# Performance work log

Hardware: AMD Instinct MI355X
Metric: run time of the kernel (lower is better)

Reference implementation:

```python
import jax, jax.numpy as jnp
import numpy as np

B, T, D = 1, 4096, 2048
NUM_HEADS, NUM_KV_HEADS, HEAD_DIM = 16, 8, 128
QUERY_PRE_ATTN_SCALAR = HEAD_DIM ** -0.5
SOFT_CAP = 50.0
WINDOW = 1024
ROPE_BASE = 10000.0
ROPE_SCALE = 1.0
K_MASK = -2.3819763e+38


def apply_rope(x, positions, head_dim, max_wavelength=ROPE_BASE, scale_factor=ROPE_SCALE):
    # x: [B, T, N, H], positions: [B, T]
    fraction = 2.0 * jnp.arange(head_dim // 2, dtype=jnp.float32) / head_dim
    timescale = max_wavelength ** fraction  # [H/2]
    sinusoid = positions[..., None].astype(jnp.float32) / timescale  # [B, T, H/2]
    sinusoid = (sinusoid / scale_factor)[..., None, :]  # [B, T, 1, H/2]
    sin, cos = jnp.sin(sinusoid), jnp.cos(sinusoid)
    first, second = jnp.split(x, 2, axis=-1)
    out = jnp.concatenate([first * cos - second * sin,
                           second * cos + first * sin], axis=-1)
    return out.astype(x.dtype)


def setup_inputs() -> dict:
    key = jax.random.key(0)
    ks = jax.random.split(key, 4)
    x = jax.random.normal(ks[0], (B, T, D), dtype=jnp.float32)
    segment_pos = jnp.broadcast_to(jnp.arange(T, dtype=jnp.int32), (B, T))
    # causal mask [B, T, S]
    attn_mask = jnp.broadcast_to(
        jnp.tril(jnp.ones((T, T), dtype=jnp.bool_)), (B, T, T))
    q_w = jax.random.normal(ks[1], (NUM_HEADS, D, HEAD_DIM), dtype=jnp.float32) * 0.02
    kv_w = jax.random.normal(ks[2], (2, NUM_KV_HEADS, D, HEAD_DIM), dtype=jnp.float32) * 0.02
    o_w = jax.random.normal(ks[3], (NUM_HEADS, HEAD_DIM, D), dtype=jnp.float32) * 0.02
    return {"x": x, "segment_pos": segment_pos, "attn_mask": attn_mask,
            "q_w": q_w, "kv_w": kv_w, "o_w": o_w}


def reference(x, segment_pos, attn_mask, q_w, kv_w, o_w):
    # Projections (GQA: separate q and kv einsums)
    q = jnp.einsum('BTD,NDH->BTNH', x, q_w)          # [B,T,N,H]
    k = jnp.einsum('BSD,KDH->BSKH', x, kv_w[0])      # [B,S,K,H]
    v = jnp.einsum('BSD,KDH->BSKH', x, kv_w[1])      # [B,S,K,H]

    q = apply_rope(q, segment_pos, HEAD_DIM)
    q = q * QUERY_PRE_ATTN_SCALAR
    k = apply_rope(k, segment_pos, HEAD_DIM)

    num_groups = NUM_HEADS // NUM_KV_HEADS
    qg = q.reshape(B, T, NUM_KV_HEADS, num_groups, HEAD_DIM)
    logits = jnp.einsum('BTKGH,BSKH->BTKGS', qg, k)
    logits = logits.reshape(B, T, NUM_HEADS, -1)     # [B,T,N,S]

    # soft cap
    logits = jnp.tanh(logits / SOFT_CAP) * SOFT_CAP

    # sliding-window mask combined with causal mask
    all_ones = jnp.ones_like(attn_mask)
    sliding = jnp.triu(all_ones, -WINDOW + 1) * jnp.tril(all_ones, WINDOW - 1)
    mask = sliding * attn_mask                       # [B,T,S] bool

    padded = jnp.where(mask[:, :, None, :], logits, K_MASK)
    probs = jax.nn.softmax(padded, axis=-1).astype(k.dtype)

    probs_g = probs.reshape(B, T, NUM_KV_HEADS, num_groups, -1)
    encoded = jnp.einsum('BTKGS,BSKH->BTKGH', probs_g, v)
    encoded = encoded.reshape(B, T, NUM_HEADS, HEAD_DIM)

    attn_output = jnp.einsum('BTNH,NHD->BTD', encoded, o_w)
    return attn_output
```

## Files before the change

### kernel.cpp

```cpp
#include <hip/hip_runtime.h>
#include <hip/hip_bf16.h>
#include <math.h>

typedef __attribute__((ext_vector_type(8))) short short8;
typedef __attribute__((ext_vector_type(8))) unsigned short ushort8;
typedef __attribute__((ext_vector_type(4))) float f32x4;

#define T_SEQ 4096
#define D_MODEL 2048
#define N_HEADS 16
#define N_KV 8
#define HEAD_DIM 128
#define QSCALE 0.08838834764831845f

__device__ __forceinline__ float bf2f(unsigned short u) {
  union { unsigned int i; float f; } x; x.i = ((unsigned int)u) << 16; return x.f;
}
__device__ __forceinline__ unsigned short f2bf(float f) {
  union { float f; unsigned int i; } x; x.f = f;
  unsigned int i = x.i;
  unsigned int r = i + 0x7fffu + ((i >> 16) & 1u);
  return (unsigned short)(r >> 16);
}

__global__ __launch_bounds__(256) void prep_kernel(const float* __restrict__ x,
                                                   unsigned short* __restrict__ xb,
                                                   const int* __restrict__ segpos,
                                                   float2* __restrict__ tab) {
  int b = blockIdx.x;
  if (b < 4096) {
    int idx = b * 256 + threadIdx.x;
    const float4* p = reinterpret_cast<const float4*>(x) + (size_t)idx * 2;
    float4 a = p[0], c = p[1];
    ushort8 o;
    o[0] = f2bf(a.x); o[1] = f2bf(a.y); o[2] = f2bf(a.z); o[3] = f2bf(a.w);
    o[4] = f2bf(c.x); o[5] = f2bf(c.y); o[6] = f2bf(c.z); o[7] = f2bf(c.w);
    reinterpret_cast<ushort8*>(xb)[idx] = o;
  } else {
    int idx = (b - 4096) * 256 + threadIdx.x;
    int t = idx >> 6, i = idx & 63;
    float pos = (float)segpos[t];
    float ts = powf(10000.f, (float)(2 * i) / 128.f);
    float ang = pos / ts;
    tab[idx] = make_float2(sinf(ang), cosf(ang));
  }
}

__global__ __launch_bounds__(256) void wqkv_transpose_kernel(const float* __restrict__ q_w,
                                                             const float* __restrict__ kv_w,
                                                             unsigned short* __restrict__ Wt) {
  __shared__ float tile[32][33];
  int z = blockIdx.z;
  const float* src = (z < 16) ? q_w + (size_t)z * 2048 * 128
                              : kv_w + (size_t)(z - 16) * 2048 * 128;
  unsigned short* dst = Wt + (size_t)z * 128 * 2048;
  int c0 = blockIdx.x * 32, r0 = blockIdx.y * 32;
  int tx = threadIdx.x & 31, ty = threadIdx.x >> 5;
#pragma unroll
  for (int i = 0; i < 4; ++i)
    tile[ty + i * 8][tx] = src[(size_t)(r0 + ty + i * 8) * 128 + c0 + tx];
  __syncthreads();
#pragma unroll
  for (int i = 0; i < 4; ++i)
    dst[(size_t)(c0 + ty + i * 8) * 2048 + r0 + tx] = f2bf(tile[tx][ty + i * 8]);
}

__global__ __launch_bounds__(256) void ow_transpose_kernel(const float* __restrict__ src,
                                                           unsigned short* __restrict__ dst) {
  __shared__ float tile[32][33];
  int c0 = blockIdx.x * 32, r0 = blockIdx.y * 32;
  int tx = threadIdx.x & 31, ty = threadIdx.x >> 5;
#pragma unroll
  for (int i = 0; i < 4; ++i)
    tile[ty + i * 8][tx] = src[(size_t)(r0 + ty + i * 8) * 2048 + c0 + tx];
  __syncthreads();
#pragma unroll
  for (int i = 0; i < 4; ++i)
    dst[(size_t)(c0 + ty + i * 8) * 2048 + r0 + tx] = f2bf(tile[tx][ty + i * 8]);
}

#define G2L(gp, lp)                                                           \
  __builtin_amdgcn_global_load_lds(                                           \
      (const __attribute__((address_space(1))) void*)(gp),                    \
      (__attribute__((address_space(3))) void*)(lp), 16, 0, 0)
#define GBAR() asm volatile("s_barrier" ::: "memory")
#define VMW(n) asm volatile("s_waitcnt vmcnt(" #n ")" ::: "memory")

template <int OUT_BF16, int NHB>
__global__ __launch_bounds__(512, 2) void gemm256_kernel(const unsigned short* __restrict__ A,
                                                         const unsigned short* __restrict__ Bt,
                                                         void* __restrict__ Cout,
                                                         int M, int N, int K) {
  constexpr int NW = 2 * NHB;
  extern __shared__ unsigned short smem[];
  unsigned short* ldsA = smem;
  unsigned short* ldsB = smem + 32768;
  const int tid = threadIdx.x;
  const int lane = tid & 63, wave = tid >> 6;
  const int wm = wave >> 2, wn = wave & 3;
  const int lr = lane & 15, lg = lane >> 4;
  const int swz = (lr & 7) << 3;
  const int c0s = (lg * 8) ^ swz;
  const int c1s = (32 + lg * 8) ^ swz;

  int id = blockIdx.y * gridDim.x + blockIdx.x;
  int nb = gridDim.x * gridDim.y;
  int sw = (id & 7) * (nb >> 3) + (id >> 3);
  const long brow = (long)(sw / gridDim.x) * 256;
  const long bcol = (long)(sw % gridDim.x) * (128 * NHB);

  const unsigned short* Ag = A + brow * K;
  const unsigned short* Bg = Bt + bcol * K;

  const int r0 = tid >> 3;
  const int cs = ((tid & 7) * 8) ^ ((r0 & 7) << 3);

#define ST_A(tt, b, a)                                                        \
  { G2L(Ag + (size_t)((a) * 128 + r0) * K + (size_t)(tt) * 64 + cs,           \
        ldsA + (b) * 16384 + (a) * 8192 + tid * 8);                           \
    G2L(Ag + (size_t)((a) * 128 + r0 + 64) * K + (size_t)(tt) * 64 + cs,      \
        ldsA + (b) * 16384 + (a) * 8192 + 4096 + tid * 8); }
#define ST_B(tt, b, h)                                                        \
  { G2L(Bg + (size_t)((h) * 128 + r0) * K + (size_t)(tt) * 64 + cs,           \
        ldsB + (b) * 8192 * NHB + (h) * 8192 + tid * 8);                      \
    G2L(Bg + (size_t)((h) * 128 + r0 + 64) * K + (size_t)(tt) * 64 + cs,      \
        ldsB + (b) * 8192 * NHB + (h) * 8192 + 4096 + tid * 8); }

  f32x4 acc[8][NW] = {};
  short8 bf[NW][2];
  short8 af[4];

#define RD_B(b)                                                               \
  { const unsigned short* pb = ldsB + (b) * 8192 * NHB + wn * 2048 * NHB;     \
    _Pragma("unroll")                                                         \
    for (int n = 0; n < NW; ++n) {                                            \
      bf[n][0] = *(const short8*)(pb + (n * 16 + lr) * 64 + c0s);             \
      bf[n][1] = *(const short8*)(pb + (n * 16 + lr) * 64 + c1s);             \
    } }
#define RD_A(b, mb)                                                           \
  { const unsigned short* pa = ldsA + (b) * 16384 + wm * 8192;                \
    af[0] = *(const short8*)(pa + ((mb) * 16 + lr) * 64 + c0s);               \
    af[1] = *(const short8*)(pa + ((mb) * 16 + lr) * 64 + c1s);               \
    af[2] = *(const short8*)(pa + ((mb) * 16 + 16 + lr) * 64 + c0s);          \
    af[3] = *(const short8*)(pa + ((mb) * 16 + 16 + lr) * 64 + c1s); }
#define MFMA2(mb)                                                             \
  { __builtin_amdgcn_s_setprio(1);                                            \
    _Pragma("unroll")                                                         \
    for (int n = 0; n < NW; ++n) {                                            \
      acc[mb][n]     = __builtin_amdgcn_mfma_f32_16x16x32_bf16(af[0], bf[n][0], acc[mb][n], 0, 0, 0);     \
      acc[mb][n]     = __builtin_amdgcn_mfma_f32_16x16x32_bf16(af[1], bf[n][1], acc[mb][n], 0, 0, 0);     \
      acc[mb + 1][n] = __builtin_amdgcn_mfma_f32_16x16x32_bf16(af[2], bf[n][0], acc[mb + 1][n], 0, 0, 0); \
      acc[mb + 1][n] = __builtin_amdgcn_mfma_f32_16x16x32_bf16(af[3], bf[n][1], acc[mb + 1][n], 0, 0, 0); \
    }                                                                         \
    __builtin_amdgcn_s_setprio(0); }

  ST_B(0, 0, 0);
  if constexpr (NHB == 2) ST_B(0, 0, 1);
  ST_A(0, 0, 0); ST_A(0, 0, 1);
  ST_B(1, 1, 0);
  if constexpr (NHB == 2) ST_B(1, 1, 1);
  if constexpr (NHB == 2) { VMW(4); } else { VMW(2); }
  ST_A(1, 1, 0); ST_A(1, 1, 1);
  GBAR();

  const int NT = K >> 6;
  for (int j = 0; j < (NT >> 1); ++j) {
    const int t2 = 2 * j + 2, t3 = 2 * j + 3;
    const bool s2 = t2 < NT, s3 = t3 < NT;
    RD_B(0); RD_A(0, 0);
    if (s2) ST_B(t2, 0, 0);
    GBAR(); MFMA2(0); GBAR();
    RD_A(0, 2);
    if constexpr (NHB == 2) { if (s2) ST_B(t2, 0, 1); }
    GBAR(); MFMA2(2); GBAR();
    RD_A(0, 4);
    GBAR(); MFMA2(4); GBAR();
    RD_A(0, 6);
    if (s2) {
      if constexpr (NHB == 2) { VMW(4); } else { VMW(2); }
      ST_A(t2, 0, 0); ST_A(t2, 0, 1);
    } else { VMW(0); }
    GBAR(); MFMA2(6); GBAR();
    RD_B(1); RD_A(1, 0);
    if (s3) ST_B(t3, 1, 0);
    GBAR(); MFMA2(0); GBAR();
    RD_A(1, 2);
    if constexpr (NHB == 2) { if (s3) ST_B(t3, 1, 1); }
    GBAR(); MFMA2(2); GBAR();
    RD_A(1, 4);
    GBAR(); MFMA2(4); GBAR();
    RD_A(1, 6);
    if (s3) {
      if constexpr (NHB == 2) { VMW(4); } else { VMW(2); }
      ST_A(t3, 1, 0); ST_A(t3, 1, 1);
    } else { VMW(0); }
    GBAR(); MFMA2(6); GBAR();
  }

#undef ST_A
#undef ST_B
#undef RD_A
#undef RD_B
#undef MFMA2

#pragma unroll
  for (int m = 0; m < 8; ++m) {
#pragma unroll
    for (int i = 0; i < 4; ++i) {
      long row = brow + wm * 128 + m * 16 + lg * 4 + i;
#pragma unroll
      for (int n = 0; n < NW; ++n) {
        long col = bcol + wn * (32 * NHB) + n * 16 + lr;
        if (OUT_BF16)
          ((unsigned short*)Cout)[row * N + col] = f2bf(acc[m][n][i]);
        else
          ((float*)Cout)[row * N + col] = acc[m][n][i];
      }
    }
  }
}

__global__ __launch_bounds__(256) void rope_vt_kernel(const unsigned short* __restrict__ raw,
                                                      const float2* __restrict__ tab,
                                                      unsigned short* __restrict__ Qb,
                                                      unsigned short* __restrict__ Kb,
                                                      unsigned short* __restrict__ Vt) {
  __shared__ unsigned short tile[32][33];
  int b = blockIdx.x;
  if (b < 3072) {
    int gid = b * 256 + threadIdx.x;
    int j = gid & 7;
    int rem = gid >> 3;
    int hs = rem % 24;
    int t = rem / 24;
    int i0 = j * 8;
    float sv[8], cv[8];
    const float2* tp = tab + t * 64 + i0;
#pragma unroll
    for (int q = 0; q < 8; ++q) { float2 sc2 = tp[q]; sv[q] = sc2.x; cv[q] = sc2.y; }
    if (hs < 16) {
      const unsigned short* p = raw + (size_t)t * 4096 + hs * 128 + i0;
      ushort8 a = *(const ushort8*)p;
      ushort8 c = *(const ushort8*)(p + 64);
      ushort8 o1, o2;
#pragma unroll
      for (int q = 0; q < 8; ++q) {
        float fa = bf2f(a[q]), fb = bf2f(c[q]);
        o1[q] = f2bf((fa * cv[q] - fb * sv[q]) * QSCALE);
        o2[q] = f2bf((fb * cv[q] + fa * sv[q]) * QSCALE);
      }
      unsigned short* qp = Qb + ((size_t)hs * T_SEQ + t) * 128 + i0;
      *(ushort8*)qp = o1;
      *(ushort8*)(qp + 64) = o2;
    } else {
      int kn = hs - 16;
      const unsigned short* p = raw + (size_t)t * 4096 + 2048 + kn * 128 + i0;
      ushort8 a = *(const ushort8*)p;
      ushort8 c = *(const ushort8*)(p + 64);
      ushort8 o1, o2;
#pragma unroll
      for (int q = 0; q < 8; ++q) {
        float fa = bf2f(a[q]), fb = bf2f(c[q]);
        o1[q] = f2bf(fa * cv[q] - fb * sv[q]);
        o2[q] = f2bf(fb * cv[q] + fa * sv[q]);
      }
      unsigned short* kp = Kb + ((size_t)kn * T_SEQ + t) * 128 + i0;
      *(ushort8*)kp = o1;
      *(ushort8*)(kp + 64) = o2;
    }
  } else {
    int id = b - 3072;
    int bx = id & 3, by = (id >> 2) & 127, bz = id >> 9;
    const unsigned short* src = raw + 3072 + (size_t)bz * 128;
    unsigned short* dst = Vt + (size_t)bz * 128 * 4096;
    int c0 = bx * 32, r0 = by * 32;
    int tx = threadIdx.x & 31, ty = threadIdx.x >> 5;
#pragma unroll
    for (int i = 0; i < 4; ++i)
      tile[ty + i * 8][tx] = src[(size_t)(r0 + ty + i * 8) * 4096 + c0 + tx];
    __syncthreads();
#pragma unroll
    for (int i = 0; i < 4; ++i)
      dst[(size_t)(c0 + ty + i * 8) * 4096 + r0 + tx] = tile[tx][ty + i * 8];
  }
}

__global__ __launch_bounds__(256, 4) void attn_kernel(const unsigned short* __restrict__ Qb,
                                                      const unsigned short* __restrict__ Kb,
                                                      const unsigned short* __restrict__ Vt,
                                                      unsigned short* __restrict__ enc) {
  __shared__ unsigned short Ks[64][128];
  __shared__ unsigned short Vs[128][64];
  __shared__ unsigned short Ps[4][16][72];
  int rawb = blockIdx.y * 64 + blockIdx.x;
  int lin = (rawb & 7) * 128 + (rawb >> 3);
  const int h = lin >> 6;
  const int qb0 = (lin & 63) * 64;
  const int kvh = h >> 1;
  const int tid = threadIdx.x, lane = tid & 63, wave = tid >> 6;
  const int qw = qb0 + wave * 16;
  const int lr = lane & 15, lg = lane >> 4;
  const int sw = (lr & 7) << 3;

  short8 aq[4];
  {
    const unsigned short* qp = Qb + ((size_t)h * T_SEQ + qw + lr) * 128 + lg * 8;
#pragma unroll
    for (int c = 0; c < 4; ++c) aq[c] = *(const short8*)(qp + c * 32);
  }
  f32x4 acc[8] = {};
  float lsum = 0.f;

  const int s_lo = (qb0 - 1023) > 0 ? (qb0 - 1023) : 0;
  const int kb_lo = s_lo >> 6, kb_hi = (qb0 + 63) >> 6;

  const int rK = tid >> 4;
  const int cpK = (tid & 15) * 8;
  const int colK = cpK ^ ((rK & 7) << 3);
  const int rV = tid >> 3;
  const int cpV = (tid & 7) * 8;
  const int colV = cpV ^ ((rV & 7) << 3);
  const unsigned short* kgb = Kb + ((size_t)kvh * T_SEQ + rK) * 128 + colK;
  const unsigned short* vgb = Vt + ((size_t)kvh * 128 + rV) * T_SEQ + colV;

  ushort8 kr[4], vr[4];
  {
    const int s0g = kb_lo * 64;
#pragma unroll
    for (int j = 0; j < 4; ++j) {
      kr[j] = *(const ushort8*)(kgb + (size_t)(s0g + j * 16) * 128);
      vr[j] = *(const ushort8*)(vgb + (size_t)(j * 32) * T_SEQ + s0g);
    }
  }

  const int qg = qw + lr;
  for (int kb = kb_lo; kb <= kb_hi; ++kb) {
    const int s0g = kb * 64;
    __syncthreads();
#pragma unroll
    for (int j = 0; j < 4; ++j) {
      *(ushort8*)&Ks[rK + j * 16][cpK] = kr[j];
      *(ushort8*)&Vs[rV + j * 32][cpV] = vr[j];
    }
    __syncthreads();
    if (kb < kb_hi) {
      const int sn = s0g + 64;
#pragma unroll
      for (int j = 0; j < 4; ++j) {
        kr[j] = *(const ushort8*)(kgb + (size_t)(sn + j * 16) * 128);
        vr[j] = *(const ushort8*)(vgb + (size_t)(j * 32) * T_SEQ + sn);
      }
    }
    if (s0g > qw + 15 || s0g + 63 < qw - 1023) continue;
    const bool interior = (s0g + 63 <= qw) && (s0g >= qw - 1008);

    f32x4 sT[4] = {};
    __builtin_amdgcn_s_setprio(1);
#pragma unroll
    for (int st = 0; st < 4; ++st) {
      const int krow = st * 16 + lr;
#pragma unroll
      for (int c = 0; c < 4; ++c) {
        short8 kf = *(const short8*)&Ks[krow][(c * 32 + lg * 8) ^ sw];
        sT[st] = __builtin_amdgcn_mfma_f32_16x16x32_bf16(kf, aq[c], sT[st], 0, 0, 0);
      }
    }
    __builtin_amdgcn_s_setprio(0);
#pragma unroll
    for (int st = 0; st < 4; ++st) {
      float p[4];
#pragma unroll
      for (int r = 0; r < 4; ++r) {
        float s = sT[st][r];
        float sl = s * 1.44269504f;
        float z2 = s * s * 4.0e-4f;
        float e = sl * (15.f + z2) * __builtin_amdgcn_rcpf(fmaf(z2, 6.f, 15.f));
        if (!interior) {
          int sg = s0g + st * 16 + lg * 4 + r;
          e = ((unsigned)(qg - sg) <= 1023u) ? e : -__builtin_inff();
        }
        float pv;
        asm("v_exp_f32 %0, %1" : "=v"(pv) : "v"(e));
        lsum += pv;
        p[r] = pv;
      }
      unsigned u0, u1;
      asm("v_cvt_pk_bf16_f32 %0, %1, %2" : "=v"(u0) : "v"(p[0]), "v"(p[1]));
      asm("v_cvt_pk_bf16_f32 %0, %1, %2" : "=v"(u1) : "v"(p[2]), "v"(p[3]));
      uint2 w; w.x = u0; w.y = u1;
      *(uint2*)&Ps[wave][lr][st * 16 + lg * 4] = w;
    }
    short8 pa0 = *(const short8*)&Ps[wave][lr][lg * 8];
    short8 pa1 = *(const short8*)&Ps[wave][lr][32 + lg * 8];
    __builtin_amdgcn_s_setprio(1);
#pragma unroll
    for (int d0 = 0; d0 < 8; ++d0) {
      const int vrow = d0 * 16 + lr;
      short8 bv0 = *(const short8*)&Vs[vrow][(lg * 8) ^ sw];
      short8 bv1 = *(const short8*)&Vs[vrow][(32 + lg * 8) ^ sw];
      acc[d0] = __builtin_amdgcn_mfma_f32_16x16x32_bf16(pa0, bv0, acc[d0], 0, 0, 0);
      acc[d0] = __builtin_amdgcn_mfma_f32_16x16x32_bf16(pa1, bv1, acc[d0], 0, 0, 0);
    }
    __builtin_amdgcn_s_setprio(0);
  }

  float l = lsum;
  l += __shfl_xor(l, 16);
  l += __shfl_xor(l, 32);
#pragma unroll
  for (int r = 0; r < 4; ++r) {
    float lt = __shfl(l, lg * 4 + r);
    float inv = __builtin_amdgcn_rcpf(lt);
    int row = qw + lg * 4 + r;
    unsigned short* op = enc + (size_t)row * D_MODEL + h * 128 + lr;
#pragma unroll
    for (int d0 = 0; d0 < 8; ++d0) op[d0 * 16] = f2bf(acc[d0][r] * inv);
  }
}

extern "C" void kernel_launch(void* const* d_in, const int* in_sizes, int n_in,
                              void* d_out, int out_size, void* d_ws, size_t ws_size,
                              hipStream_t stream) {
  const float* x = (const float*)d_in[0];
  const int* segpos = (const int*)d_in[1];
  const float* q_w = (const float*)d_in[3];
  const float* kv_w = (const float*)d_in[4];
  const float* o_w = (const float*)d_in[5];
  float* out = (float*)d_out;
  char* ws = (char*)d_ws;

  const size_t OFF_XB = 0;
  const size_t OFF_WT = OFF_XB + 16777216;
  const size_t OFF_RAW = OFF_WT + 16777216;
  const size_t OFF_KB = OFF_RAW + 33554432;
  const size_t OFF_VT = OFF_KB + 8388608;
  const size_t OFF_TAB = OFF_VT + 8388608;
  unsigned short* xb = (unsigned short*)(ws + OFF_XB);
  unsigned short* Wt = (unsigned short*)(ws + OFF_WT);
  unsigned short* raw = (unsigned short*)(ws + OFF_RAW);
  unsigned short* Kb = (unsigned short*)(ws + OFF_KB);
  unsigned short* Vt = (unsigned short*)(ws + OFF_VT);
  float2* tab = (float2*)(ws + OFF_TAB);
  unsigned short* o_wt = xb;
  unsigned short* Qb = Wt;
  unsigned short* enc = raw;

  hipFuncSetAttribute((const void*)(gemm256_kernel<1, 2>),
                      hipFuncAttributeMaxDynamicSharedMemorySize, 131072);
  hipFuncSetAttribute((const void*)(gemm256_kernel<0, 1>),
                      hipFuncAttributeMaxDynamicSharedMemorySize, 98304);

  prep_kernel<<<dim3(5120), dim3(256), 0, stream>>>(x, xb, segpos, tab);
  wqkv_transpose_kernel<<<dim3(4, 64, 32), dim3(256), 0, stream>>>(q_w, kv_w, Wt);
  gemm256_kernel<1, 2><<<dim3(16, 16), dim3(512), 131072, stream>>>(xb, Wt, (void*)raw, 4096, 4096, 2048);
  ow_transpose_kernel<<<dim3(64, 64), dim3(256), 0, stream>>>(o_w, o_wt);
  rope_vt_kernel<<<dim3(7168), dim3(256), 0, stream>>>(raw, tab, Qb, Kb, Vt);
  attn_kernel<<<dim3(64, 16), dim3(256), 0, stream>>>(Qb, Kb, Vt, enc);
  gemm256_kernel<0, 1><<<dim3(16, 16), dim3(512), 98304, stream>>>(enc, o_wt, (void*)out, 4096, 2048, 2048);
}
```

Before: 211.9 us.

## Enlarge attention query tile per block and retile GEMM to 128x256

The attention kernel now runs 512-thread blocks over 256 query rows, and each wave handles two 16-row query groups. That lets each K/V fragment read from LDS feed twice as many MFMAs and cuts redundant K/V global loads across blocks. The GEMM template switches its parameter from N-halves to M-halves, so the output projection uses 128x256 tiles with a restructured pipeline that adds explicit lgkmcnt waits. The softcap and exp math is also vectorised into float2 form. The cost is higher register pressure and fewer, larger attention blocks (256), which may leave the load less balanced across CUs.

```diff
diff --git a/kernel.cpp b/kernel.cpp
--- a/kernel.cpp
+++ b/kernel.cpp
@@ -5,6 +5,7 @@
 typedef __attribute__((ext_vector_type(8))) short short8;
 typedef __attribute__((ext_vector_type(8))) unsigned short ushort8;
 typedef __attribute__((ext_vector_type(4))) float f32x4;
+typedef __attribute__((ext_vector_type(2))) float f32x2;
 
 #define T_SEQ 4096
 #define D_MODEL 2048
@@ -85,16 +86,18 @@
       (__attribute__((address_space(3))) void*)(lp), 16, 0, 0)
 #define GBAR() asm volatile("s_barrier" ::: "memory")
 #define VMW(n) asm volatile("s_waitcnt vmcnt(" #n ")" ::: "memory")
-
-template <int OUT_BF16, int NHB>
+#define LGKM0()                                                               \
+  { asm volatile("s_waitcnt lgkmcnt(0)" ::: "memory");                        \
+    __builtin_amdgcn_sched_barrier(0); }
+
+template <int OUT_BF16, int MHB>
 __global__ __launch_bounds__(512, 2) void gemm256_kernel(const unsigned short* __restrict__ A,
                                                          const unsigned short* __restrict__ Bt,
                                                          void* __restrict__ Cout,
                                                          int M, int N, int K) {
-  constexpr int NW = 2 * NHB;
   extern __shared__ unsigned short smem[];
   unsigned short* ldsA = smem;
-  unsigned short* ldsB = smem + 32768;
+  unsigned short* ldsB = smem + 2 * MHB * 8192;
   const int tid = threadIdx.x;
   const int lane = tid & 63, wave = tid >> 6;
   const int wm = wave >> 2, wn = wave & 3;
@@ -106,8 +109,8 @@
   int id = blockIdx.y * gridDim.x + blockIdx.x;
   int nb = gridDim.x * gridDim.y;
   int sw = (id & 7) * (nb >> 3) + (id >> 3);
-  const long brow = (long)(sw / gridDim.x) * 256;
-  const long bcol = (long)(sw % gridDim.x) * (128 * NHB);
+  const long brow = (long)(sw / gridDim.x) * (128 * MHB);
+  const long bcol = (long)(sw % gridDim.x) * 256;
 
   const unsigned short* Ag = A + brow * K;
   const unsigned short* Bg = Bt + bcol * K;
@@ -117,28 +120,28 @@
 
 #define ST_A(tt, b, a)                                                        \
   { G2L(Ag + (size_t)((a) * 128 + r0) * K + (size_t)(tt) * 64 + cs,           \
-        ldsA + (b) * 16384 + (a) * 8192 + tid * 8);                           \
+        ldsA + (b) * (MHB * 8192) + (a) * 8192 + tid * 8);                    \
     G2L(Ag + (size_t)((a) * 128 + r0 + 64) * K + (size_t)(tt) * 64 + cs,      \
-        ldsA + (b) * 16384 + (a) * 8192 + 4096 + tid * 8); }
+        ldsA + (b) * (MHB * 8192) + (a) * 8192 + 4096 + tid * 8); }
 #define ST_B(tt, b, h)                                                        \
   { G2L(Bg + (size_t)((h) * 128 + r0) * K + (size_t)(tt) * 64 + cs,           \
-        ldsB + (b) * 8192 * NHB + (h) * 8192 + tid * 8);                      \
+        ldsB + (b) * 16384 + (h) * 8192 + tid * 8);                           \
     G2L(Bg + (size_t)((h) * 128 + r0 + 64) * K + (size_t)(tt) * 64 + cs,      \
-        ldsB + (b) * 8192 * NHB + (h) * 8192 + 4096 + tid * 8); }
-
-  f32x4 acc[8][NW] = {};
-  short8 bf[NW][2];
+        ldsB + (b) * 16384 + (h) * 8192 + 4096 + tid * 8); }
+
+  f32x4 acc[4 * MHB][4] = {};
+  short8 bf[4][2];
   short8 af[4];
 
 #define RD_B(b)                                                               \
-  { const unsigned short* pb = ldsB + (b) * 8192 * NHB + wn * 2048 * NHB;     \
+  { const unsigned short* pb = ldsB + (b) * 16384 + wn * 4096;                \
     _Pragma("unroll")                                                         \
-    for (int n = 0; n < NW; ++n) {                                            \
+    for (int n = 0; n < 4; ++n) {                                             \
       bf[n][0] = *(const short8*)(pb + (n * 16 + lr) * 64 + c0s);             \
       bf[n][1] = *(const short8*)(pb + (n * 16 + lr) * 64 + c1s);             \
     } }
 #define RD_A(b, mb)                                                           \
-  { const unsigned short* pa = ldsA + (b) * 16384 + wm * 8192;                \
+  { const unsigned short* pa = ldsA + (b) * (MHB * 8192) + wm * (MHB * 4096); \
     af[0] = *(const short8*)(pa + ((mb) * 16 + lr) * 64 + c0s);               \
     af[1] = *(const short8*)(pa + ((mb) * 16 + lr) * 64 + c1s);               \
     af[2] = *(const short8*)(pa + ((mb) * 16 + 16 + lr) * 64 + c0s);          \
@@ -146,7 +149,7 @@
 #define MFMA2(mb)                                                             \
   { __builtin_amdgcn_s_setprio(1);                                            \
     _Pragma("unroll")                                                         \
-    for (int n = 0; n < NW; ++n) {                                            \
+    for (int n = 0; n < 4; ++n) {                                             \
       acc[mb][n]     = __builtin_amdgcn_mfma_f32_16x16x32_bf16(af[0], bf[n][0], acc[mb][n], 0, 0, 0);     \
       acc[mb][n]     = __builtin_amdgcn_mfma_f32_16x16x32_bf16(af[1], bf[n][1], acc[mb][n], 0, 0, 0);     \
       acc[mb + 1][n] = __builtin_amdgcn_mfma_f32_16x16x32_bf16(af[2], bf[n][0], acc[mb + 1][n], 0, 0, 0); \
@@ -154,49 +157,47 @@
     }                                                                         \
     __builtin_amdgcn_s_setprio(0); }
 
-  ST_B(0, 0, 0);
-  if constexpr (NHB == 2) ST_B(0, 0, 1);
-  ST_A(0, 0, 0); ST_A(0, 0, 1);
-  ST_B(1, 1, 0);
-  if constexpr (NHB == 2) ST_B(1, 1, 1);
-  if constexpr (NHB == 2) { VMW(4); } else { VMW(2); }
-  ST_A(1, 1, 0); ST_A(1, 1, 1);
+  ST_B(0, 0, 0); ST_B(0, 0, 1);
+  ST_A(0, 0, 0);
+  if constexpr (MHB == 2) ST_A(0, 0, 1);
+  ST_B(1, 1, 0); ST_B(1, 1, 1);
+  if constexpr (MHB == 2) { VMW(4); } else { VMW(4); }
+  ST_A(1, 1, 0);
+  if constexpr (MHB == 2) ST_A(1, 1, 1);
   GBAR();
+
+#define TILE(b, tn, sflag)                                                    \
+  { RD_B(b); RD_A(b, 0);                                                      \
+    LGKM0(); GBAR();                \
+    if (sflag) ST_B(tn, b, 0);                 \
+    MFMA2(0); GBAR();                                                         \
+    if constexpr (MHB == 1) {                                                 \
+      RD_A(b, 2);                                                             \
+      LGKM0(); GBAR();                          \
+      if (sflag) { ST_B(tn, b, 1); VMW(4); ST_A(tn, b, 0); }                  \
+      else       { VMW(0); }                                                  \
+      MFMA2(2); GBAR();                                                       \
+    } else {                                                                  \
+      RD_A(b, 2);                                                             \
+      if (sflag) ST_B(tn, b, 1);         \
+      GBAR(); MFMA2(2); GBAR();                                               \
+      RD_A(b, 4);                                                             \
+      GBAR(); MFMA2(4); GBAR();                                               \
+      RD_A(b, 6);                                                             \
+      LGKM0(); GBAR();                          \
+      if (sflag) { VMW(4); ST_A(tn, b, 0); ST_A(tn, b, 1); }                  \
+      else       { VMW(0); }                                                  \
+      MFMA2(6); GBAR();                                                       \
+    } }
 
   const int NT = K >> 6;
   for (int j = 0; j < (NT >> 1); ++j) {
     const int t2 = 2 * j + 2, t3 = 2 * j + 3;
-    const bool s2 = t2 < NT, s3 = t3 < NT;
-    RD_B(0); RD_A(0, 0);
-    if (s2) ST_B(t2, 0, 0);
-    GBAR(); MFMA2(0); GBAR();
-    RD_A(0, 2);
-    if constexpr (NHB == 2) { if (s2) ST_B(t2, 0, 1); }
-    GBAR(); MFMA2(2); GBAR();
-    RD_A(0, 4);
-    GBAR(); MFMA2(4); GBAR();
-    RD_A(0, 6);
-    if (s2) {
-      if constexpr (NHB == 2) { VMW(4); } else { VMW(2); }
-      ST_A(t2, 0, 0); ST_A(t2, 0, 1);
-    } else { VMW(0); }
-    GBAR(); MFMA2(6); GBAR();
-    RD_B(1); RD_A(1, 0);
-    if (s3) ST_B(t3, 1, 0);
-    GBAR(); MFMA2(0); GBAR();
-    RD_A(1, 2);
-    if constexpr (NHB == 2) { if (s3) ST_B(t3, 1, 1); }
-    GBAR(); MFMA2(2); GBAR();
-    RD_A(1, 4);
-    GBAR(); MFMA2(4); GBAR();
-    RD_A(1, 6);
-    if (s3) {
-      if constexpr (NHB == 2) { VMW(4); } else { VMW(2); }
-      ST_A(t3, 1, 0); ST_A(t3, 1, 1);
-    } else { VMW(0); }
-    GBAR(); MFMA2(6); GBAR();
-  }
-
+    TILE(0, t2, (t2 < NT));
+    TILE(1, t3, (t3 < NT));
+  }
+
+#undef TILE
 #undef ST_A
 #undef ST_B
 #undef RD_A
@@ -204,13 +205,13 @@
 #undef MFMA2
 
 #pragma unroll
-  for (int m = 0; m < 8; ++m) {
+  for (int m = 0; m < 4 * MHB; ++m) {
 #pragma unroll
     for (int i = 0; i < 4; ++i) {
-      long row = brow + wm * 128 + m * 16 + lg * 4 + i;
-#pragma unroll
-      for (int n = 0; n < NW; ++n) {
-        long col = bcol + wn * (32 * NHB) + n * 16 + lr;
+      long row = brow + wm * (64 * MHB) + m * 16 + lg * 4 + i;
+#pragma unroll
+      for (int n = 0; n < 4; ++n) {
+        long col = bcol + wn * 64 + n * 16 + lr;
         if (OUT_BF16)
           ((unsigned short*)Cout)[row * N + col] = f2bf(acc[m][n][i]);
         else
@@ -285,34 +286,37 @@
   }
 }
 
-__global__ __launch_bounds__(256, 4) void attn_kernel(const unsigned short* __restrict__ Qb,
+__global__ __launch_bounds__(512, 2) void attn_kernel(const unsigned short* __restrict__ Qb,
                                                       const unsigned short* __restrict__ Kb,
                                                       const unsigned short* __restrict__ Vt,
                                                       unsigned short* __restrict__ enc) {
   __shared__ unsigned short Ks[64][128];
   __shared__ unsigned short Vs[128][64];
-  __shared__ unsigned short Ps[4][16][72];
-  int rawb = blockIdx.y * 64 + blockIdx.x;
-  int lin = (rawb & 7) * 128 + (rawb >> 3);
-  const int h = lin >> 6;
-  const int qb0 = (lin & 63) * 64;
+  __shared__ unsigned short Ps[8][32][72];
+  int rawb = blockIdx.x;
+  int lin = (rawb & 7) * 32 + (rawb >> 3);
+  const int h = lin >> 4;
+  const int qb0 = (lin & 15) * 256;
   const int kvh = h >> 1;
   const int tid = threadIdx.x, lane = tid & 63, wave = tid >> 6;
-  const int qw = qb0 + wave * 16;
+  const int qw = qb0 + wave * 32;
   const int lr = lane & 15, lg = lane >> 4;
   const int sw = (lr & 7) << 3;
-
-  short8 aq[4];
-  {
-    const unsigned short* qp = Qb + ((size_t)h * T_SEQ + qw + lr) * 128 + lg * 8;
-#pragma unroll
-    for (int c = 0; c < 4; ++c) aq[c] = *(const short8*)(qp + c * 32);
-  }
-  f32x4 acc[8] = {};
-  float lsum = 0.f;
+  const int ck0 = (lg * 8) ^ sw, ck1 = (32 + lg * 8) ^ sw;
+  const int ck2 = (64 + lg * 8) ^ sw, ck3 = (96 + lg * 8) ^ sw;
+
+  short8 aq[2][4];
+#pragma unroll
+  for (int g = 0; g < 2; ++g) {
+    const unsigned short* qp = Qb + ((size_t)h * T_SEQ + qw + g * 16 + lr) * 128 + lg * 8;
+#pragma unroll
+    for (int c = 0; c < 4; ++c) aq[g][c] = *(const short8*)(qp + c * 32);
+  }
+  f32x4 acc[2][8] = {};
+  float lsum[2] = {0.f, 0.f};
 
   const int s_lo = (qb0 - 1023) > 0 ? (qb0 - 1023) : 0;
-  const int kb_lo = s_lo >> 6, kb_hi = (qb0 + 63) >> 6;
+  const int kb_lo = s_lo >> 6, kb_hi = (qb0 + 255) >> 6;
 
   const int rK = tid >> 4;
   const int cpK = (tid & 15) * 8;
@@ -323,98 +327,121 @@
   const unsigned short* kgb = Kb + ((size_t)kvh * T_SEQ + rK) * 128 + colK;
   const unsigned short* vgb = Vt + ((size_t)kvh * 128 + rV) * T_SEQ + colV;
 
-  ushort8 kr[4], vr[4];
+  ushort8 kr0, kr1, vr0, vr1;
   {
     const int s0g = kb_lo * 64;
-#pragma unroll
-    for (int j = 0; j < 4; ++j) {
-      kr[j] = *(const ushort8*)(kgb + (size_t)(s0g + j * 16) * 128);
-      vr[j] = *(const ushort8*)(vgb + (size_t)(j * 32) * T_SEQ + s0g);
-    }
-  }
-
-  const int qg = qw + lr;
+    kr0 = *(const ushort8*)(kgb + (size_t)s0g * 128);
+    kr1 = *(const ushort8*)(kgb + (size_t)(s0g + 32) * 128);
+    vr0 = *(const ushort8*)(vgb + s0g);
+    vr1 = *(const ushort8*)(vgb + (size_t)64 * T_SEQ + s0g);
+  }
+
+  const int qg0 = qw + lr, qg1 = qw + 16 + lr;
   for (int kb = kb_lo; kb <= kb_hi; ++kb) {
     const int s0g = kb * 64;
     __syncthreads();
-#pragma unroll
-    for (int j = 0; j < 4; ++j) {
-      *(ushort8*)&Ks[rK + j * 16][cpK] = kr[j];
-      *(ushort8*)&Vs[rV + j * 32][cpV] = vr[j];
-    }
+    *(ushort8*)&Ks[rK][cpK] = kr0;
+    *(ushort8*)&Ks[rK + 32][cpK] = kr1;
+    *(ushort8*)&Vs[rV][cpV] = vr0;
+    *(ushort8*)&Vs[rV + 64][cpV] = vr1;
     __syncthreads();
     if (kb < kb_hi) {
       const int sn = s0g + 64;
-#pragma unroll
-      for (int j = 0; j < 4; ++j) {
-        kr[j] = *(const ushort8*)(kgb + (size_t)(sn + j * 16) * 128);
-        vr[j] = *(const ushort8*)(vgb + (size_t)(j * 32) * T_SEQ + sn);
+      kr0 = *(const ushort8*)(kgb + (size_t)sn * 128);
+      kr1 = *(const ushort8*)(kgb + (size_t)(sn + 32) * 128);
+      vr0 = *(const ushort8*)(vgb + sn);
+      vr1 = *(const ushort8*)(vgb + (size_t)64 * T_SEQ + sn);
+    }
+    if (s0g > qw + 31 || s0g + 63 < qw - 1023) continue;
+    const bool interior = (s0g + 63 <= qw) && (s0g >= qw - 992);
+
+    f32x4 sT0[4] = {}, sT1[4] = {};
+    __builtin_amdgcn_s_setprio(1);
+#pragma unroll
+    for (int st = 0; st < 4; ++st) {
+      const unsigned short* kp = &Ks[st * 16 + lr][0];
+      short8 k0 = *(const short8*)(kp + ck0);
+      short8 k1 = *(const short8*)(kp + ck1);
+      short8 k2 = *(const short8*)(kp + ck2);
+      short8 k3 = *(const short8*)(kp + ck3);
+      sT0[st] = __builtin_amdgcn_mfma_f32_16x16x32_bf16(k0, aq[0][0], sT0[st], 0, 0, 0);
+      sT1[st] = __builtin_amdgcn_mfma_f32_16x16x32_bf16(k0, aq[1][0], sT1[st], 0, 0, 0);
+      sT0[st] = __builtin_amdgcn_mfma_f32_16x16x32_bf16(k1, aq[0][1], sT0[st], 0, 0, 0);
+      sT1[st] = __builtin_amdgcn_mfma_f32_16x16x32_bf16(k1, aq[1][1], sT1[st], 0, 0, 0);
+      sT0[st] = __builtin_amdgcn_mfma_f32_16x16x32_bf16(k2, aq[0][2], sT0[st], 0, 0, 0);
+      sT1[st] = __builtin_amdgcn_mfma_f32_16x16x32_bf16(k2, aq[1][2], sT1[st], 0, 0, 0);
+      sT0[st] = __builtin_amdgcn_mfma_f32_16x16x32_bf16(k3, aq[0][3], sT0[st], 0, 0, 0);
+      sT1[st] = __builtin_amdgcn_mfma_f32_16x16x32_bf16(k3, aq[1][3], sT1[st], 0, 0, 0);
+    }
+    __builtin_amdgcn_s_setprio(0);
+
+#pragma unroll
+    for (int g = 0; g < 2; ++g) {
+      const f32x4* sTg = g ? sT1 : sT0;
+      const int qgg = g ? qg1 : qg0;
+#pragma unroll
+      for (int st = 0; st < 4; ++st) {
+        f32x4 svv = sTg[st];
+        f32x2 sa, sb;
+        sa[0] = svv[0]; sa[1] = svv[1]; sb[0] = svv[2]; sb[1] = svv[3];
+        f32x2 ua = sa * sa, ub = sb * sb;
+        f32x2 numa = ua * 4.0e-4f + 15.f, numb = ub * 4.0e-4f + 15.f;
+        f32x2 dena = ua * 2.4e-3f + 15.f, denb = ub * 2.4e-3f + 15.f;
+        f32x2 ra, rb;
+        ra[0] = __builtin_amdgcn_rcpf(dena[0]); ra[1] = __builtin_amdgcn_rcpf(dena[1]);
+        rb[0] = __builtin_amdgcn_rcpf(denb[0]); rb[1] = __builtin_amdgcn_rcpf(denb[1]);
+        f32x2 ea = (sa * 1.44269504f) * numa * ra;
+        f32x2 eb = (sb * 1.44269504f) * numb * rb;
+        float e[4] = {ea[0], ea[1], eb[0], eb[1]};
+        float p[4];
+#pragma unroll
+        for (int r = 0; r < 4; ++r) {
+          if (!interior) {
+            int sg = s0g + st * 16 + lg * 4 + r;
+            e[r] = ((unsigned)(qgg - sg) <= 1023u) ? e[r] : -__builtin_inff();
+          }
+          asm("v_exp_f32 %0, %1" : "=v"(p[r]) : "v"(e[r]));
+        }
+        lsum[g] += (p[0] + p[1]) + (p[2] + p[3]);
+        unsigned u0, u1;
+        asm("v_cvt_pk_bf16_f32 %0, %1, %2" : "=v"(u0) : "v"(p[0]), "v"(p[1]));
+        asm("v_cvt_pk_bf16_f32 %0, %1, %2" : "=v"(u1) : "v"(p[2]), "v"(p[3]));
+        uint2 w; w.x = u0; w.y = u1;
+        *(uint2*)&Ps[wave][g * 16 + lr][st * 16 + lg * 4] = w;
       }
     }
-    if (s0g > qw + 15 || s0g + 63 < qw - 1023) continue;
-    const bool interior = (s0g + 63 <= qw) && (s0g >= qw - 1008);
-
-    f32x4 sT[4] = {};
+    short8 pa00 = *(const short8*)&Ps[wave][lr][lg * 8];
+    short8 pa01 = *(const short8*)&Ps[wave][lr][32 + lg * 8];
+    short8 pa10 = *(const short8*)&Ps[wave][16 + lr][lg * 8];
+    short8 pa11 = *(const short8*)&Ps[wave][16 + lr][32 + lg * 8];
     __builtin_amdgcn_s_setprio(1);
 #pragma unroll
-    for (int st = 0; st < 4; ++st) {
-      const int krow = st * 16 + lr;
-#pragma unroll
-      for (int c = 0; c < 4; ++c) {
-        short8 kf = *(const short8*)&Ks[krow][(c * 32 + lg * 8) ^ sw];
-        sT[st] = __builtin_amdgcn_mfma_f32_16x16x32_bf16(kf, aq[c], sT[st], 0, 0, 0);
-      }
+    for (int d0 = 0; d0 < 8; ++d0) {
+      const unsigned short* vp = &Vs[d0 * 16 + lr][0];
+      short8 bv0 = *(const short8*)(vp + ((lg * 8) ^ sw));
+      short8 bv1 = *(const short8*)(vp + ((32 + lg * 8) ^ sw));
+      acc[0][d0] = __builtin_amdgcn_mfma_f32_16x16x32_bf16(pa00, bv0, acc[0][d0], 0, 0, 0);
+      acc[1][d0] = __builtin_amdgcn_mfma_f32_16x16x32_bf16(pa10, bv0, acc[1][d0], 0, 0, 0);
+      acc[0][d0] = __builtin_amdgcn_mfma_f32_16x16x32_bf16(pa01, bv1, acc[0][d0], 0, 0, 0);
+      acc[1][d0] = __builtin_amdgcn_mfma_f32_16x16x32_bf16(pa11, bv1, acc[1][d0], 0, 0, 0);
     }
     __builtin_amdgcn_s_setprio(0);
-#pragma unroll
-    for (int st = 0; st < 4; ++st) {
-      float p[4];
-#pragma unroll
-      for (int r = 0; r < 4; ++r) {
-        float s = sT[st][r];
-        float sl = s * 1.44269504f;
-        float z2 = s * s * 4.0e-4f;
-        float e = sl * (15.f + z2) * __builtin_amdgcn_rcpf(fmaf(z2, 6.f, 15.f));
-        if (!interior) {
-          int sg = s0g + st * 16 + lg * 4 + r;
-          e = ((unsigned)(qg - sg) <= 1023u) ? e : -__builtin_inff();
-        }
-        float pv;
-        asm("v_exp_f32 %0, %1" : "=v"(pv) : "v"(e));
-        lsum += pv;
-        p[r] = pv;
-      }
-      unsigned u0, u1;
-      asm("v_cvt_pk_bf16_f32 %0, %1, %2" : "=v"(u0) : "v"(p[0]), "v"(p[1]));
-      asm("v_cvt_pk_bf16_f32 %0, %1, %2" : "=v"(u1) : "v"(p[2]), "v"(p[3]));
-      uint2 w; w.x = u0; w.y = u1;
-      *(uint2*)&Ps[wave][lr][st * 16 + lg * 4] = w;
-    }
-    short8 pa0 = *(const short8*)&Ps[wave][lr][lg * 8];
-    short8 pa1 = *(const short8*)&Ps[wave][lr][32 + lg * 8];
-    __builtin_amdgcn_s_setprio(1);
-#pragma unroll
-    for (int d0 = 0; d0 < 8; ++d0) {
-      const int vrow = d0 * 16 + lr;
-      short8 bv0 = *(const short8*)&Vs[vrow][(lg * 8) ^ sw];
-      short8 bv1 = *(const short8*)&Vs[vrow][(32 + lg * 8) ^ sw];
-      acc[d0] = __builtin_amdgcn_mfma_f32_16x16x32_bf16(pa0, bv0, acc[d0], 0, 0, 0);
-      acc[d0] = __builtin_amdgcn_mfma_f32_16x16x32_bf16(pa1, bv1, acc[d0], 0, 0, 0);
-    }
-    __builtin_amdgcn_s_setprio(0);
-  }
-
-  float l = lsum;
-  l += __shfl_xor(l, 16);
-  l += __shfl_xor(l, 32);
-#pragma unroll
-  for (int r = 0; r < 4; ++r) {
-    float lt = __shfl(l, lg * 4 + r);
-    float inv = __builtin_amdgcn_rcpf(lt);
-    int row = qw + lg * 4 + r;
-    unsigned short* op = enc + (size_t)row * D_MODEL + h * 128 + lr;
-#pragma unroll
-    for (int d0 = 0; d0 < 8; ++d0) op[d0 * 16] = f2bf(acc[d0][r] * inv);
+  }
+
+#pragma unroll
+  for (int g = 0; g < 2; ++g) {
+    float l = lsum[g];
+    l += __shfl_xor(l, 16);
+    l += __shfl_xor(l, 32);
+#pragma unroll
+    for (int r = 0; r < 4; ++r) {
+      float lt = __shfl(l, lg * 4 + r);
+      float inv = __builtin_amdgcn_rcpf(lt);
+      int row = qw + g * 16 + lg * 4 + r;
+      unsigned short* op = enc + (size_t)row * D_MODEL + h * 128 + lr;
+#pragma unroll
+      for (int d0 = 0; d0 < 8; ++d0) op[d0 * 16] = f2bf(acc[g][d0][r] * inv);
+    }
   }
 }
 
@@ -455,6 +482,6 @@
   gemm256_kernel<1, 2><<<dim3(16, 16), dim3(512), 131072, stream>>>(xb, Wt, (void*)raw, 4096, 4096, 2048);
   ow_transpose_kernel<<<dim3(64, 64), dim3(256), 0, stream>>>(o_w, o_wt);
   rope_vt_kernel<<<dim3(7168), dim3(256), 0, stream>>>(raw, tab, Qb, Kb, Vt);
-  attn_kernel<<<dim3(64, 16), dim3(256), 0, stream>>>(Qb, Kb, Vt, enc);
-  gemm256_kernel<0, 1><<<dim3(16, 16), dim3(512), 98304, stream>>>(enc, o_wt, (void*)out, 4096, 2048, 2048);
-}
+  attn_kernel<<<dim3(256), dim3(512), 0, stream>>>(Qb, Kb, Vt, enc);
+  gemm256_kernel<0, 1><<<dim3(8, 32), dim3(512), 98304, stream>>>(enc, o_wt, (void*)out, 4096, 2048, 2048);
+}
```

Result: faster. 202.7 us (-4.4%).
